# Optimization experiments

Measured on AMD Instinct MI355X. Metric: run time of the kernel, lower is better.

The kernel has to match this reference:

```python
import jax, jax.numpy as jnp
import numpy as np

B, N_BLOCK, D_MODEL = 4096, 64, 256


def setup_inputs() -> dict:
    key = jax.random.key(0)
    k1, k2 = jax.random.split(key)
    h = jax.random.normal(k1, (B, N_BLOCK, D_MODEL), dtype=jnp.float32)
    # xavier_normal_ for square [d, d]: std = sqrt(2/(d+d)) = 1/sqrt(d)
    W_a = jax.random.normal(k2, (D_MODEL, D_MODEL), dtype=jnp.float32) / jnp.sqrt(
        jnp.float32(D_MODEL))
    b_a = jnp.zeros((N_BLOCK, D_MODEL), dtype=jnp.float32)
    return {"h": h, "W_a": W_a, "b_a": b_a}


def reference(h, W_a, b_a):
    # h: [B, n_block, d_model]
    # scores = tanh(h @ W_a + b_a): [B, n_block, d_model]
    s = jnp.tanh(jnp.einsum("bnd,de->bne", h, W_a) + b_a)
    # Original applies Softmax(dim=1) to a [1, n_block, d_model] chunk,
    # i.e. normalization is over the n_block axis.
    a = jax.nn.softmax(s, axis=1)
    # elementwise weight then full sum per block -> [B, n_block]
    return jnp.sum(a * h, axis=2)
```

## Files before the change

kernel.cpp:

```cpp
#include <hip/hip_runtime.h>
#include <hip/hip_bf16.h>

#define BATCH 4096
#define NB    64
#define DM    256
#define KSW   8
#define KST   10

typedef __bf16 bf16x8 __attribute__((ext_vector_type(8)));
typedef float  f32x4  __attribute__((ext_vector_type(4)));

union Frag16 { uint4 u; bf16x8 b; ushort s[8]; };
union Pk2    { __hip_bfloat162 v; unsigned u; };

__device__ __forceinline__ ushort f2bf(float x) {
    unsigned u = __float_as_uint(x);
    return (ushort)((u + 0x7FFFu + ((u >> 16) & 1u)) >> 16);
}
__device__ __forceinline__ unsigned pk2(float a, float b) {
    Pk2 p; p.v = __float22bfloat162_rn(make_float2(a, b));
    return p.u;
}
__device__ __forceinline__ float bf2f(ushort u) {
    return __uint_as_float(((unsigned)u) << 16);
}

__global__ void swizzle_WB(const float* __restrict__ W, const float* __restrict__ ba,
                           ushort* __restrict__ Wf) {
    int idx  = blockIdx.x * 256 + threadIdx.x;
    int lane = idx & 63;
    int g    = idx >> 6;
    int et   = g / KST;
    int ks   = g % KST;
    int e    = et * 16 + (lane & 15);
    int r0   = (ks < KSW) ? ks * 32 : (ks - KSW) * 32;
    r0 += ((lane >> 4) << 3);
    const float* src = (ks < KSW) ? W : ba;
    Frag16 f;
#pragma unroll
    for (int j = 0; j < 8; ++j)
        f.s[j] = f2bf(src[(r0 + j) * DM + e]);
    reinterpret_cast<uint4*>(Wf)[idx] = f.u;
}

__global__ __launch_bounds__(256, 4) void aspect_attn(
    const float*  __restrict__ h,
    const ushort* __restrict__ Wf,
    float*        __restrict__ out)
{
    __shared__ __align__(16) ushort Hs[2048 * 8];
    __shared__ float op[4][NB];

    const int tid  = threadIdx.x;
    const int wave = tid >> 6;
    const int lane = tid & 63;
    const int quad = lane >> 4;
    const int l15  = lane & 15;
    const int b    = blockIdx.x;

    const float* hb = h + (size_t)b * (NB * DM);

#pragma unroll
    for (int it = 0; it < 8; ++it) {
        int slot = it * 256 + tid;
        int f    = slot >> 6;
        int row  = ((f >> 3) << 4) | l15;
        int k0   = ((f & 7) << 5) | (quad << 3);
        const f32x4* p = reinterpret_cast<const f32x4*>(hb + row * DM + k0);
        f32x4 a = p[0], c = p[1];
        uint4 o;
        o.x = pk2(a.x, a.y); o.y = pk2(a.z, a.w);
        o.z = pk2(c.x, c.y); o.w = pk2(c.z, c.w);
        reinterpret_cast<uint4*>(Hs)[slot] = o;
    }
    __syncthreads();

    f32x4 acc[4][4];
#pragma unroll
    for (int mt = 0; mt < 4; ++mt)
#pragma unroll
        for (int nt = 0; nt < 4; ++nt) {
            f32x4 z = {0.f, 0.f, 0.f, 0.f};
            acc[mt][nt] = z;
        }

    const uint4* WfB = reinterpret_cast<const uint4*>(Wf);
    const uint4* HsB = reinterpret_cast<const uint4*>(Hs);

#pragma unroll
    for (int ks = 0; ks < KSW; ++ks) {
        Frag16 af[4], bfr[4];
#pragma unroll
        for (int mt = 0; mt < 4; ++mt)
            af[mt].u = HsB[(mt * 8 + ks) * 64 + lane];
#pragma unroll
        for (int nt = 0; nt < 4; ++nt)
            bfr[nt].u = WfB[((wave * 4 + nt) * KST + ks) * 64 + lane];
#pragma unroll
        for (int mt = 0; mt < 4; ++mt)
#pragma unroll
            for (int nt = 0; nt < 4; ++nt)
                acc[mt][nt] = __builtin_amdgcn_mfma_f32_16x16x32_bf16(
                    af[mt].b, bfr[nt].b, acc[mt][nt], 0, 0, 0);
    }
#pragma unroll
    for (int kx = 0; kx < 2; ++kx) {
        Frag16 af[4], bfr[4];
#pragma unroll
        for (int nt = 0; nt < 4; ++nt)
            bfr[nt].u = WfB[((wave * 4 + nt) * KST + KSW + kx) * 64 + lane];
        const int kb = kx * 32 + quad * 8;
#pragma unroll
        for (int mt = 0; mt < 4; ++mt) {
            int d = (mt * 16 + l15) - kb;
#pragma unroll
            for (int j = 0; j < 8; ++j)
                af[mt].s[j] = (d == j) ? (ushort)0x3F80 : (ushort)0;
        }
#pragma unroll
        for (int mt = 0; mt < 4; ++mt)
#pragma unroll
            for (int nt = 0; nt < 4; ++nt)
                acc[mt][nt] = __builtin_amdgcn_mfma_f32_16x16x32_bf16(
                    af[mt].b, bfr[nt].b, acc[mt][nt], 0, 0, 0);
    }

#pragma unroll
    for (int mt = 0; mt < 4; ++mt)
#pragma unroll
        for (int nt = 0; nt < 4; ++nt)
#pragma unroll
            for (int r = 0; r < 4; ++r) {
                float x = acc[mt][nt][r];
                float e = __expf(-2.f * fabsf(x));
                float t = (1.f - e) * __builtin_amdgcn_rcpf(1.f + e);
                acc[mt][nt][r] = copysignf(t, x);
            }

#pragma unroll
    for (int nt = 0; nt < 4; ++nt) {
        float ls = 0.f;
#pragma unroll
        for (int mt = 0; mt < 4; ++mt)
#pragma unroll
            for (int r = 0; r < 4; ++r) {
                float p = __expf(acc[mt][nt][r]);
                acc[mt][nt][r] = p;
                ls += p;
            }
        ls += __shfl_xor(ls, 16, 64);
        ls += __shfl_xor(ls, 32, 64);
        float inv = __builtin_amdgcn_rcpf(ls);
#pragma unroll
        for (int mt = 0; mt < 4; ++mt)
#pragma unroll
            for (int r = 0; r < 4; ++r)
                acc[mt][nt][r] *= inv;
    }

    const int colb = wave * 64;
#pragma unroll
    for (int mt = 0; mt < 4; ++mt)
#pragma unroll
        for (int r = 0; r < 4; ++r) {
            const int row  = mt * 16 + quad * 4 + r;
            const int ridx = mt * 4096 + (quad * 4 + r) * 8;
            float s = 0.f;
#pragma unroll
            for (int nt = 0; nt < 4; ++nt) {
                int col  = colb + nt * 16 + l15;
                int coff = (col >> 5) * 512 + ((col >> 3) & 3) * 128 + (col & 7);
                s += acc[mt][nt][r] * bf2f(Hs[ridx + coff]);
            }
#pragma unroll
            for (int m = 1; m < 16; m <<= 1)
                s += __shfl_xor(s, m, 64);
            if (l15 == 0) op[wave][row] = s;
        }
    __syncthreads();

    if (tid < NB)
        out[(size_t)b * NB + tid] = op[0][tid] + op[1][tid] + op[2][tid] + op[3][tid];
}

extern "C" void kernel_launch(void* const* d_in, const int* in_sizes, int n_in,
                              void* d_out, int out_size, void* d_ws, size_t ws_size,
                              hipStream_t stream) {
    const float* h  = (const float*)d_in[0];
    const float* W  = (const float*)d_in[1];
    const float* ba = (const float*)d_in[2];
    float* out = (float*)d_out;
    ushort* Wf = (ushort*)d_ws;

    swizzle_WB<<<40, 256, 0, stream>>>(W, ba, Wf);
    aspect_attn<<<BATCH, 256, 0, stream>>>(h, Wf, out);
}
```

Baseline: 407.9 us.

## Make attention kernel persistent with register-resident W and double-buffered h prefetch

The kernel becomes persistent: 256 blocks of 512 threads each loop over 16 batches. Each wave keeps its slice of the swizzled W/bias fragments in registers for the whole loop, and the next batch's h is loaded into registers while the current batch computes, then written into a second LDS buffer. The tanh+exp pair is folded algebraically into two exps, and the row reduction uses DPP instead of shuffles. This aims to remove repeated W global loads and hide h load latency, at the cost of fewer resident blocks and higher register pressure.

```diff
diff --git a/kernel.cpp b/kernel.cpp
--- a/kernel.cpp
+++ b/kernel.cpp
@@ -6,6 +6,8 @@
 #define DM    256
 #define KSW   8
 #define KST   10
+#define PBLK  256
+#define NTIL  (BATCH / PBLK)
 
 typedef __bf16 bf16x8 __attribute__((ext_vector_type(8)));
 typedef float  f32x4  __attribute__((ext_vector_type(4)));
@@ -23,6 +25,11 @@
 }
 __device__ __forceinline__ float bf2f(ushort u) {
     return __uint_as_float(((unsigned)u) << 16);
+}
+template<int CTRL>
+__device__ __forceinline__ float dpp_add(float s) {
+    int t = __builtin_amdgcn_update_dpp(0, __float_as_int(s), CTRL, 0xF, 0xF, true);
+    return s + __int_as_float(t);
 }
 
 __global__ void swizzle_WB(const float* __restrict__ W, const float* __restrict__ ba,
@@ -43,144 +50,169 @@
     reinterpret_cast<uint4*>(Wf)[idx] = f.u;
 }
 
-__global__ __launch_bounds__(256, 4) void aspect_attn(
+__global__ __launch_bounds__(512, 2) void aspect_attn(
     const float*  __restrict__ h,
     const ushort* __restrict__ Wf,
     float*        __restrict__ out)
 {
-    __shared__ __align__(16) ushort Hs[2048 * 8];
-    __shared__ float op[4][NB];
+    __shared__ __align__(16) ushort Hs[2][16384];
+    __shared__ float op[8][NB];
 
     const int tid  = threadIdx.x;
     const int wave = tid >> 6;
     const int lane = tid & 63;
     const int quad = lane >> 4;
     const int l15  = lane & 15;
-    const int b    = blockIdx.x;
-
-    const float* hb = h + (size_t)b * (NB * DM);
-
-#pragma unroll
-    for (int it = 0; it < 8; ++it) {
-        int slot = it * 256 + tid;
-        int f    = slot >> 6;
-        int row  = ((f >> 3) << 4) | l15;
-        int k0   = ((f & 7) << 5) | (quad << 3);
-        const f32x4* p = reinterpret_cast<const f32x4*>(hb + row * DM + k0);
-        f32x4 a = p[0], c = p[1];
-        uint4 o;
-        o.x = pk2(a.x, a.y); o.y = pk2(a.z, a.w);
-        o.z = pk2(c.x, c.y); o.w = pk2(c.z, c.w);
-        reinterpret_cast<uint4*>(Hs)[slot] = o;
+    const int bid  = blockIdx.x;
+
+    const uint4* WfB = reinterpret_cast<const uint4*>(Wf);
+    Frag16 wf[2][KST];
+#pragma unroll
+    for (int nt = 0; nt < 2; ++nt)
+#pragma unroll
+        for (int ks = 0; ks < KST; ++ks)
+            wf[nt][ks].u = WfB[(((wave << 1) | nt) * KST + ks) * 64 + lane];
+
+    const int sk0 = (wave << 5) | (quad << 3);
+
+    f32x4 pa[4], pc[4];
+
+    {
+        const float* hb = h + (size_t)bid * (NB * DM);
+#pragma unroll
+        for (int it = 0; it < 4; ++it) {
+            const f32x4* p = reinterpret_cast<const f32x4*>(hb + (it * 16 + l15) * DM + sk0);
+            pa[it] = p[0]; pc[it] = p[1];
+        }
+#pragma unroll
+        for (int it = 0; it < 4; ++it) {
+            uint4 o;
+            o.x = pk2(pa[it].x, pa[it].y); o.y = pk2(pa[it].z, pa[it].w);
+            o.z = pk2(pc[it].x, pc[it].y); o.w = pk2(pc[it].z, pc[it].w);
+            reinterpret_cast<uint4*>(Hs[0])[(it * 8 + wave) * 64 + lane] = o;
+        }
     }
     __syncthreads();
 
-    f32x4 acc[4][4];
-#pragma unroll
-    for (int mt = 0; mt < 4; ++mt)
-#pragma unroll
-        for (int nt = 0; nt < 4; ++nt) {
-            f32x4 z = {0.f, 0.f, 0.f, 0.f};
-            acc[mt][nt] = z;
-        }
-
-    const uint4* WfB = reinterpret_cast<const uint4*>(Wf);
-    const uint4* HsB = reinterpret_cast<const uint4*>(Hs);
-
-#pragma unroll
-    for (int ks = 0; ks < KSW; ++ks) {
-        Frag16 af[4], bfr[4];
+#pragma unroll 2
+    for (int t = 0; t < NTIL; ++t) {
+        const int cur = t & 1;
+
+        if (t + 1 < NTIL) {
+            const float* hb = h + (size_t)((t + 1) * PBLK + bid) * (NB * DM);
+#pragma unroll
+            for (int it = 0; it < 4; ++it) {
+                const f32x4* p = reinterpret_cast<const f32x4*>(hb + (it * 16 + l15) * DM + sk0);
+                pa[it] = p[0]; pc[it] = p[1];
+            }
+        }
+
+        f32x4 acc[4][2];
 #pragma unroll
         for (int mt = 0; mt < 4; ++mt)
-            af[mt].u = HsB[(mt * 8 + ks) * 64 + lane];
-#pragma unroll
-        for (int nt = 0; nt < 4; ++nt)
-            bfr[nt].u = WfB[((wave * 4 + nt) * KST + ks) * 64 + lane];
+#pragma unroll
+            for (int nt = 0; nt < 2; ++nt) {
+                f32x4 z = {0.f, 0.f, 0.f, 0.f};
+                acc[mt][nt] = z;
+            }
+
+        const uint4* HsB = reinterpret_cast<const uint4*>(Hs[cur]);
+#pragma unroll
+        for (int ks = 0; ks < KSW; ++ks) {
+            Frag16 af[4];
+#pragma unroll
+            for (int mt = 0; mt < 4; ++mt)
+                af[mt].u = HsB[(mt * 8 + ks) * 64 + lane];
+#pragma unroll
+            for (int mt = 0; mt < 4; ++mt)
+#pragma unroll
+                for (int nt = 0; nt < 2; ++nt)
+                    acc[mt][nt] = __builtin_amdgcn_mfma_f32_16x16x32_bf16(
+                        af[mt].b, wf[nt][ks].b, acc[mt][nt], 0, 0, 0);
+        }
+#pragma unroll
+        for (int kx = 0; kx < 2; ++kx) {
+            Frag16 af[4];
+            const int kb = kx * 32 + (quad << 3);
+#pragma unroll
+            for (int mt = 0; mt < 4; ++mt) {
+                int d = (mt * 16 + l15) - kb;
+#pragma unroll
+                for (int j = 0; j < 8; ++j)
+                    af[mt].s[j] = (d == j) ? (ushort)0x3F80 : (ushort)0;
+            }
+#pragma unroll
+            for (int mt = 0; mt < 4; ++mt)
+#pragma unroll
+                for (int nt = 0; nt < 2; ++nt)
+                    acc[mt][nt] = __builtin_amdgcn_mfma_f32_16x16x32_bf16(
+                        af[mt].b, wf[nt][KSW + kx].b, acc[mt][nt], 0, 0, 0);
+        }
+
+#pragma unroll
+        for (int nt = 0; nt < 2; ++nt) {
+            float ls = 0.f;
+#pragma unroll
+            for (int mt = 0; mt < 4; ++mt)
+#pragma unroll
+                for (int r = 0; r < 4; ++r) {
+                    float x = acc[mt][nt][r];
+                    float u = __expf(2.f * x);
+                    float p = __expf(-2.f * __builtin_amdgcn_rcpf(u + 1.f));
+                    acc[mt][nt][r] = p;
+                    ls += p;
+                }
+            ls += __shfl_xor(ls, 16, 64);
+            ls += __shfl_xor(ls, 32, 64);
+            float inv = __builtin_amdgcn_rcpf(ls);
+#pragma unroll
+            for (int mt = 0; mt < 4; ++mt)
+#pragma unroll
+                for (int r = 0; r < 4; ++r)
+                    acc[mt][nt][r] *= inv;
+        }
+
+        const int colb = wave << 5;
+        const ushort* Hc = Hs[cur];
 #pragma unroll
         for (int mt = 0; mt < 4; ++mt)
 #pragma unroll
-            for (int nt = 0; nt < 4; ++nt)
-                acc[mt][nt] = __builtin_amdgcn_mfma_f32_16x16x32_bf16(
-                    af[mt].b, bfr[nt].b, acc[mt][nt], 0, 0, 0);
+            for (int r = 0; r < 4; ++r) {
+                const int row  = mt * 16 + (quad << 2) + r;
+                const int ridx = mt * 4096 + ((quad << 2) + r) * 8;
+                float s = 0.f;
+#pragma unroll
+                for (int nt = 0; nt < 2; ++nt) {
+                    int col  = colb + nt * 16 + l15;
+                    int coff = (col >> 5) * 512 + ((col >> 3) & 3) * 128 + (col & 7);
+                    s += acc[mt][nt][r] * bf2f(Hc[ridx + coff]);
+                }
+                s = dpp_add<0xB1>(s);
+                s = dpp_add<0x4E>(s);
+                s = dpp_add<0x141>(s);
+                s = dpp_add<0x140>(s);
+                if (l15 == 0) op[wave][row] = s;
+            }
+        __syncthreads();
+
+        if (t + 1 < NTIL) {
+#pragma unroll
+            for (int it = 0; it < 4; ++it) {
+                uint4 o;
+                o.x = pk2(pa[it].x, pa[it].y); o.y = pk2(pa[it].z, pa[it].w);
+                o.z = pk2(pc[it].x, pc[it].y); o.w = pk2(pc[it].z, pc[it].w);
+                reinterpret_cast<uint4*>(Hs[cur ^ 1])[(it * 8 + wave) * 64 + lane] = o;
+            }
+        }
+
+        if (tid < NB) {
+            float r = op[0][tid];
+#pragma unroll
+            for (int w = 1; w < 8; ++w) r += op[w][tid];
+            out[(size_t)(t * PBLK + bid) * NB + tid] = r;
+        }
+        __syncthreads();
     }
-#pragma unroll
-    for (int kx = 0; kx < 2; ++kx) {
-        Frag16 af[4], bfr[4];
-#pragma unroll
-        for (int nt = 0; nt < 4; ++nt)
-            bfr[nt].u = WfB[((wave * 4 + nt) * KST + KSW + kx) * 64 + lane];
-        const int kb = kx * 32 + quad * 8;
-#pragma unroll
-        for (int mt = 0; mt < 4; ++mt) {
-            int d = (mt * 16 + l15) - kb;
-#pragma unroll
-            for (int j = 0; j < 8; ++j)
-                af[mt].s[j] = (d == j) ? (ushort)0x3F80 : (ushort)0;
-        }
-#pragma unroll
-        for (int mt = 0; mt < 4; ++mt)
-#pragma unroll
-            for (int nt = 0; nt < 4; ++nt)
-                acc[mt][nt] = __builtin_amdgcn_mfma_f32_16x16x32_bf16(
-                    af[mt].b, bfr[nt].b, acc[mt][nt], 0, 0, 0);
-    }
-
-#pragma unroll
-    for (int mt = 0; mt < 4; ++mt)
-#pragma unroll
-        for (int nt = 0; nt < 4; ++nt)
-#pragma unroll
-            for (int r = 0; r < 4; ++r) {
-                float x = acc[mt][nt][r];
-                float e = __expf(-2.f * fabsf(x));
-                float t = (1.f - e) * __builtin_amdgcn_rcpf(1.f + e);
-                acc[mt][nt][r] = copysignf(t, x);
-            }
-
-#pragma unroll
-    for (int nt = 0; nt < 4; ++nt) {
-        float ls = 0.f;
-#pragma unroll
-        for (int mt = 0; mt < 4; ++mt)
-#pragma unroll
-            for (int r = 0; r < 4; ++r) {
-                float p = __expf(acc[mt][nt][r]);
-                acc[mt][nt][r] = p;
-                ls += p;
-            }
-        ls += __shfl_xor(ls, 16, 64);
-        ls += __shfl_xor(ls, 32, 64);
-        float inv = __builtin_amdgcn_rcpf(ls);
-#pragma unroll
-        for (int mt = 0; mt < 4; ++mt)
-#pragma unroll
-            for (int r = 0; r < 4; ++r)
-                acc[mt][nt][r] *= inv;
-    }
-
-    const int colb = wave * 64;
-#pragma unroll
-    for (int mt = 0; mt < 4; ++mt)
-#pragma unroll
-        for (int r = 0; r < 4; ++r) {
-            const int row  = mt * 16 + quad * 4 + r;
-            const int ridx = mt * 4096 + (quad * 4 + r) * 8;
-            float s = 0.f;
-#pragma unroll
-            for (int nt = 0; nt < 4; ++nt) {
-                int col  = colb + nt * 16 + l15;
-                int coff = (col >> 5) * 512 + ((col >> 3) & 3) * 128 + (col & 7);
-                s += acc[mt][nt][r] * bf2f(Hs[ridx + coff]);
-            }
-#pragma unroll
-            for (int m = 1; m < 16; m <<= 1)
-                s += __shfl_xor(s, m, 64);
-            if (l15 == 0) op[wave][row] = s;
-        }
-    __syncthreads();
-
-    if (tid < NB)
-        out[(size_t)b * NB + tid] = op[0][tid] + op[1][tid] + op[2][tid] + op[3][tid];
 }
 
 extern "C" void kernel_launch(void* const* d_in, const int* in_sizes, int n_in,
@@ -193,5 +225,5 @@
     ushort* Wf = (ushort*)d_ws;
 
     swizzle_WB<<<40, 256, 0, stream>>>(W, ba, Wf);
-    aspect_attn<<<BATCH, 256, 0, stream>>>(h, Wf, out);
-}
+    aspect_attn<<<PBLK, 512, 0, stream>>>(h, Wf, out);
+}
```

Result: faster. 366.5 us (-10.1%).
